# Optimization experiments

Hardware: AMD Instinct MI355X
Metric: run time of the kernel (lower is better)

The kernel has to match this reference:

```python
import jax, jax.numpy as jnp
import numpy as np
from jax import lax

B, S = 128, 8192
MIN_PATCH, MAX_PATCH = 2, 16
LOOKAHEAD = 8
THRESHOLD = 2.9
PAD_TOKEN = 0
VOCAB = 256
MAXP = -(-S // MIN_PATCH)  # static upper bound on #patches (torch trims to batch max; we pad+mask)


def setup_inputs() -> dict:
    key = jax.random.key(0)
    tokens = jax.random.randint(key, (B, S), 0, VOCAB, dtype=jnp.int32)
    return {"tokens": tokens}


def _entropy_all_starts(seq):
    # ent[j] = Shannon entropy (bits) of window seq[j : min(S, j + LOOKAHEAD)]
    # Using c_i = multiplicity of element i within its window:
    #   H = -(1/L) * sum_i log2(c_i / L)   (each unique value contributes c_i identical terms)
    pos = jnp.arange(S)[:, None] + jnp.arange(LOOKAHEAD)[None, :]          # [S, L]
    valid = pos < S
    w = seq[jnp.minimum(pos, S - 1)]                                       # [S, L]
    eq = (w[:, :, None] == w[:, None, :]) & valid[:, :, None] & valid[:, None, :]
    counts = eq.sum(-1).astype(jnp.float32)                                # [S, L] c_i (0 where invalid)
    L = valid.sum(-1).astype(jnp.float32)                                  # [S]
    logs = jnp.where(valid, jnp.log2(jnp.maximum(counts, 1.0) / jnp.maximum(L, 1.0)[:, None]), 0.0)
    return -logs.sum(-1) / jnp.maximum(L, 1.0)                             # [S]


def _patch_one(seq):
    ent = _entropy_all_starts(seq)
    stop = ent >= THRESHOLD
    # next_stop[j] = smallest j' >= j with stop[j'], else S (padded so next_stop[S] = S)
    vals = jnp.concatenate([jnp.where(stop, jnp.arange(S, dtype=jnp.int32), S),
                            jnp.array([S], dtype=jnp.int32)])
    next_stop = lax.associative_scan(jnp.minimum, vals, reverse=True)      # [S+1]
    i_all = jnp.arange(S, dtype=jnp.int32)
    # inner while-loop closed form: grow from min_patch until stop/seq-end/max_patch
    sizes = jnp.minimum(MAX_PATCH, next_stop[jnp.minimum(i_all + MIN_PATCH, S)] - i_all)  # [S]

    def step(i, _):
        ok = i < S
        sz = jnp.where(ok, sizes[jnp.minimum(i, S - 1)], 1)
        return i + sz, (i, sz, ok)

    _, (starts, szs, mask) = lax.scan(step, jnp.int32(0), None, length=MAXP)
    return starts, szs, mask


def reference(tokens):
    starts, szs, mask = jax.vmap(_patch_one)(tokens)                       # [B, MAXP]
    lane = jnp.arange(MAX_PATCH, dtype=jnp.int32)
    idx = starts[:, :, None] + lane[None, None, :]                         # [B, MAXP, MAX_PATCH]
    within = (lane[None, None, :] < szs[:, :, None]) & mask[:, :, None]
    g = jnp.take_along_axis(tokens, jnp.minimum(idx, S - 1).reshape(tokens.shape[0], -1), axis=1)
    patches = jnp.where(within, g.reshape(tokens.shape[0], MAXP, MAX_PATCH), PAD_TOKEN)
    return patches, mask
```

## Files before the change

### kernel.cpp

```cpp
#include <hip/hip_runtime.h>
#include <stdint.h>

#define SEQ  8192
#define NB   128
#define MAXP 4096
#define NT   512
#define RED  2
#define NCH  256
#define STS  36

__device__ __forceinline__ bool haszero8(uint64_t v) {
    return ((v - 0x0101010101010101ULL) & ~v & 0x8080808080808080ULL) != 0ULL;
}
__device__ __forceinline__ bool distinct8(uint64_t w) {
    uint64_t r1 = (w >> 8)  | (w << 56);
    uint64_t r2 = (w >> 16) | (w << 48);
    uint64_t r3 = (w >> 24) | (w << 40);
    uint64_t r4 = (w >> 32) | (w << 32);
    return !(haszero8(w ^ r1) | haszero8(w ^ r2) | haszero8(w ^ r3) | haszero8(w ^ r4));
}
__device__ __forceinline__ uint32_t pack4(int4 v) {
    return (uint32_t)(v.x & 255) | ((uint32_t)(v.y & 255) << 8) |
           ((uint32_t)(v.z & 255) << 16) | ((uint32_t)(v.w & 255) << 24);
}
__device__ __forceinline__ uint32_t bsel16(uint4 f, uint32_t b) {
    uint32_t w01 = (b & 4u) ? f.y : f.x;
    uint32_t w23 = (b & 4u) ? f.w : f.z;
    uint32_t w   = (b & 8u) ? w23 : w01;
    return (w >> ((b & 3u) << 3)) & 255u;
}
__device__ __forceinline__ uint4 comp16(uint4 g, uint4 f) {
    uint4 r;
#if __has_builtin(__builtin_amdgcn_perm)
    #define C16W(fw, out) do { \
        uint32_t sel = (fw) & 0x07070707u; \
        uint32_t lo = __builtin_amdgcn_perm(g.y, g.x, sel); \
        uint32_t hi = __builtin_amdgcn_perm(g.w, g.z, sel); \
        uint32_t m = ((fw) & 0x08080808u) >> 3; m = (m << 8) - m; \
        out = (lo & ~m) | (hi & m); } while (0)
    C16W(f.x, r.x); C16W(f.y, r.y); C16W(f.z, r.z); C16W(f.w, r.w);
    #undef C16W
#else
    #define C16B(fw, out) do { uint32_t o = 0; \
        o |= bsel16(g, (fw) & 15u); \
        o |= bsel16(g, ((fw) >> 8) & 15u) << 8; \
        o |= bsel16(g, ((fw) >> 16) & 15u) << 16; \
        o |= bsel16(g, ((fw) >> 24) & 15u) << 24; \
        out = o; } while (0)
    C16B(f.x, r.x); C16B(f.y, r.y); C16B(f.z, r.z); C16B(f.w, r.w);
    #undef C16B
#endif
    return r;
}
__device__ __forceinline__ int psize(const uint32_t* stopb, int p) {
    int bp = p + 2, w = bp >> 5;
    uint64_t comb = (uint64_t)stopb[w] | ((uint64_t)stopb[w + 1] << 32);
    uint32_t win14 = (uint32_t)(comb >> (bp & 31)) & 0x3FFFu;
    return win14 ? (2 + __builtin_ctz(win14)) : min(16, SEQ - p);
}

__global__ __launch_bounds__(NT) void ep_fused(const int* __restrict__ tokens,
                                               int* __restrict__ out) {
    __shared__ uint32_t tok32[2056];
    __shared__ uint32_t stopb[258];
    __shared__ uint16_t st_l[NCH * STS];
    __shared__ uint32_t exitf32[NCH * 4];
    __shared__ uint8_t  entry_s[NCH];
    __shared__ uint16_t pbase_s[NCH];
    __shared__ uint16_t starts_s[4100];
    __shared__ int S_s[2];

    const int bx = blockIdx.x;
    const int b = bx >> 1, qc = bx & 1;
    const int tid = threadIdx.x;

    {
        const int4* t4 = (const int4*)(tokens + (size_t)b * SEQ);
        #pragma unroll
        for (int k = 0; k < 4; ++k) { int g = k * NT + tid; tok32[g] = pack4(t4[g]); }
        if (tid < 8) tok32[2048 + tid] = 0u;
        if (tid < 2) stopb[256 + tid] = 0u;
    }
    __syncthreads();

    {
        const int base = tid * 4;
        uint64_t win = (uint64_t)tok32[base] | ((uint64_t)tok32[base + 1] << 32);
        uint32_t bits = 0;
        #pragma unroll
        for (int k = 0; k < 4; ++k) {
            uint32_t nx = tok32[base + 2 + k];
            #pragma unroll
            for (int m = 0; m < 4; ++m) {
                int j = tid * 16 + k * 4 + m;
                if (j <= SEQ - 8 && distinct8(win)) bits |= (1u << (k * 4 + m));
                win = (win >> 8) | ((uint64_t)(nx & 255u) << 56);
                nx >>= 8;
            }
        }
        uint32_t other = (uint32_t)__shfl_xor((int)bits, 1);
        if ((tid & 1) == 0) stopb[tid >> 1] = (bits & 0xFFFFu) | (other << 16);
    }
    __syncthreads();

    if (tid < NCH) {
        const int c = tid;
        const uint64_t W = (uint64_t)stopb[c] | ((uint64_t)stopb[c + 1] << 32);
        uint16_t* st = st_l + c * STS;
        const int gb = c * 32;
        #pragma unroll 4
        for (int rel = 31; rel >= 0; --rel) {
            uint32_t win14 = (uint32_t)(W >> (rel + 2)) & 0x3FFFu;
            int sz = win14 ? (2 + __builtin_ctz(win14)) : min(16, SEQ - (gb + rel));
            int nxt = rel + sz;
            int ra = (nxt < 32) ? nxt : 0;
            uint32_t sv = st[ra];
            uint32_t cont = (sv & 0xFFu) | (((sv >> 8) + 1u) << 8);
            uint32_t exitv = (uint32_t)(nxt - 32) | 0x100u;
            st[rel] = (uint16_t)((nxt >= 32) ? exitv : cont);
        }
        #pragma unroll
        for (int w = 0; w < 4; ++w) {
            uint32_t e0 = st[w * 4 + 0] & 0xFFu, e1 = st[w * 4 + 1] & 0xFFu,
                     e2 = st[w * 4 + 2] & 0xFFu, e3 = st[w * 4 + 3] & 0xFFu;
            exitf32[c * 4 + w] = e0 | (e1 << 8) | (e2 << 16) | (e3 << 24);
        }
    }
    __syncthreads();

    if (tid < 64) {
        const uint4* xf4 = (const uint4*)exitf32;
        uint4 f0 = xf4[tid * 4], f1 = xf4[tid * 4 + 1],
              f2 = xf4[tid * 4 + 2], f3 = xf4[tid * 4 + 3];
        uint4 g = comp16(f1, f0);
        g = comp16(f2, g);
        g = comp16(f3, g);
        #pragma unroll
        for (int d = 1; d < 64; d <<= 1) {
            uint4 o;
            o.x = (uint32_t)__shfl_up((int)g.x, d);
            o.y = (uint32_t)__shfl_up((int)g.y, d);
            o.z = (uint32_t)__shfl_up((int)g.z, d);
            o.w = (uint32_t)__shfl_up((int)g.w, d);
            if (tid >= d) g = comp16(g, o);
        }
        uint4 E;
        E.x = (uint32_t)__shfl_up((int)g.x, 1);
        E.y = (uint32_t)__shfl_up((int)g.y, 1);
        E.z = (uint32_t)__shfl_up((int)g.z, 1);
        E.w = (uint32_t)__shfl_up((int)g.w, 1);
        if (tid == 0) E = make_uint4(0x03020100u, 0x07060504u, 0x0B0A0908u, 0x0F0E0D0Cu);
        uint32_t e0 = E.x & 255u;
        uint32_t e1 = bsel16(f0, e0);
        uint32_t e2 = bsel16(f1, e1);
        uint32_t e3 = bsel16(f2, e2);
        entry_s[tid * 4 + 0] = (uint8_t)e0;
        entry_s[tid * 4 + 1] = (uint8_t)e1;
        entry_s[tid * 4 + 2] = (uint8_t)e2;
        entry_s[tid * 4 + 3] = (uint8_t)e3;
        int c0 = (int)(st_l[(tid * 4 + 0) * STS + (int)e0] >> 8);
        int c1 = (int)(st_l[(tid * 4 + 1) * STS + (int)e1] >> 8);
        int c2 = (int)(st_l[(tid * 4 + 2) * STS + (int)e2] >> 8);
        int c3 = (int)(st_l[(tid * 4 + 3) * STS + (int)e3] >> 8);
        int s = c0 + c1 + c2 + c3;
        int incl = s;
        #pragma unroll
        for (int d = 1; d < 64; d <<= 1) { int o = __shfl_up(incl, d); if (tid >= d) incl += o; }
        int excl = incl - s;
        pbase_s[tid * 4 + 0] = (uint16_t)excl;
        pbase_s[tid * 4 + 1] = (uint16_t)(excl + c0);
        pbase_s[tid * 4 + 2] = (uint16_t)(excl + c0 + c1);
        pbase_s[tid * 4 + 3] = (uint16_t)(excl + c0 + c1 + c2);
        if (tid == 63) S_s[0] = incl;
    }
    __syncthreads();

    if (tid < NCH) {
        int pb = (int)pbase_s[tid];
        int p = tid * 32 + (int)entry_s[tid];
        const int lim = tid * 32 + 32;
        while (p < lim) {
            starts_s[pb++] = (uint16_t)p;
            p += psize(stopb, p);
        }
    }
    {
        const int P = S_s[0];
        for (int i = P + tid; i < 4098; i += NT) starts_s[i] = (uint16_t)SEQ;
    }
    __syncthreads();

    {
        int* outp = out + (size_t)b * (MAXP * 16);
        int* outm = out + (size_t)NB * MAXP * 16 + (size_t)b * MAXP;
        const int j = tid & 3;
        #pragma unroll
        for (int it = 0; it < (MAXP / RED) / (NT / 4); ++it) {
            const int p = qc * (MAXP / RED) + it * (NT / 4) + (tid >> 2);
            const int st = (int)starts_s[p];
            const int sz = (int)starts_s[p + 1] - st;
            const int base = (st >> 2) + j;
            const uint32_t sh = (uint32_t)(st & 3) * 8u;
            uint32_t lo = tok32[base], hi = tok32[base + 1];
            uint32_t pk = (uint32_t)((((uint64_t)hi << 32) | lo) >> sh);
            int rem = sz - 4 * j;
            rem = (rem < 0) ? 0 : (rem > 4 ? 4 : rem);
            pk &= (uint32_t)((1ULL << (8 * rem)) - 1ULL);
            ((int4*)outp)[(size_t)p * 4 + j] =
                make_int4((int)(pk & 255u), (int)((pk >> 8) & 255u),
                          (int)((pk >> 16) & 255u), (int)(pk >> 24));
        }
        #pragma unroll
        for (int i = 0; i < (MAXP / RED) / NT; ++i) {
            const int p = qc * (MAXP / RED) + i * NT + tid;
            outm[p] = ((int)starts_s[p] < SEQ) ? 1 : 0;
        }
    }
}

extern "C" void kernel_launch(void* const* d_in, const int* in_sizes, int n_in,
                              void* d_out, int out_size, void* d_ws, size_t ws_size,
                              hipStream_t stream) {
    const int* tokens = (const int*)d_in[0];
    int* out = (int*)d_out;
    ep_fused<<<dim3(NB * RED), dim3(NT), 0, stream>>>(tokens, out);
}
```

Measured before the change: 21.47 us.

## Keep per-chunk patch state table in registers and vectorize mask stores

The serial 32-step backward pass over each 32-position chunk now builds its exit/count table in eight packed 32-bit registers, looked up with a select tree. This replaces dependent LDS loads and stores on every step. The exit bytes are packed with a byte-permute, and a 32-bit-packed table is written once to LDS for the later count lookup. It also drops the per-window bounds check in the stop-bit loop in favour of a single mask on the last thread, and writes the mask output as one int4 per thread. The cost is more register pressure and a fully unrolled select chain.

```diff
diff --git a/kernel.cpp b/kernel.cpp
--- a/kernel.cpp
+++ b/kernel.cpp
@@ -7,7 +7,6 @@
 #define NT   512
 #define RED  2
 #define NCH  256
-#define STS  36
 
 __device__ __forceinline__ bool haszero8(uint64_t v) {
     return ((v - 0x0101010101010101ULL) & ~v & 0x8080808080808080ULL) != 0ULL;
@@ -28,6 +27,14 @@
     uint32_t w23 = (b & 4u) ? f.w : f.z;
     uint32_t w   = (b & 8u) ? w23 : w01;
     return (w >> ((b & 3u) << 3)) & 255u;
+}
+__device__ __forceinline__ uint32_t packexit(uint32_t pa, uint32_t pb) {
+#if __has_builtin(__builtin_amdgcn_perm)
+    return __builtin_amdgcn_perm(pb, pa, 0x06040200u);
+#else
+    return (pa & 0xFFu) | (((pa >> 16) & 0xFFu) << 8) |
+           ((pb & 0xFFu) << 16) | (((pb >> 16) & 0xFFu) << 24);
+#endif
 }
 __device__ __forceinline__ uint4 comp16(uint4 g, uint4 f) {
     uint4 r;
@@ -63,7 +70,7 @@
                                                int* __restrict__ out) {
     __shared__ uint32_t tok32[2056];
     __shared__ uint32_t stopb[258];
-    __shared__ uint16_t st_l[NCH * STS];
+    __shared__ uint32_t st16[NCH * 9];
     __shared__ uint32_t exitf32[NCH * 4];
     __shared__ uint8_t  entry_s[NCH];
     __shared__ uint16_t pbase_s[NCH];
@@ -92,12 +99,12 @@
             uint32_t nx = tok32[base + 2 + k];
             #pragma unroll
             for (int m = 0; m < 4; ++m) {
-                int j = tid * 16 + k * 4 + m;
-                if (j <= SEQ - 8 && distinct8(win)) bits |= (1u << (k * 4 + m));
+                if (distinct8(win)) bits |= (1u << (k * 4 + m));
                 win = (win >> 8) | ((uint64_t)(nx & 255u) << 56);
                 nx >>= 8;
             }
         }
+        if (tid == NT - 1) bits &= 0x1FFu;
         uint32_t other = (uint32_t)__shfl_xor((int)bits, 1);
         if ((tid & 1) == 0) stopb[tid >> 1] = (bits & 0xFFFFu) | (other << 16);
     }
@@ -106,25 +113,44 @@
     if (tid < NCH) {
         const int c = tid;
         const uint64_t W = (uint64_t)stopb[c] | ((uint64_t)stopb[c + 1] << 32);
-        uint16_t* st = st_l + c * STS;
         const int gb = c * 32;
-        #pragma unroll 4
+        uint32_t p0 = 0, p1 = 0, p2 = 0, p3 = 0, p4 = 0, p5 = 0, p6 = 0, p7 = 0;
+        #pragma unroll
         for (int rel = 31; rel >= 0; --rel) {
             uint32_t win14 = (uint32_t)(W >> (rel + 2)) & 0x3FFFu;
             int sz = win14 ? (2 + __builtin_ctz(win14)) : min(16, SEQ - (gb + rel));
             int nxt = rel + sz;
-            int ra = (nxt < 32) ? nxt : 0;
-            uint32_t sv = st[ra];
-            uint32_t cont = (sv & 0xFFu) | (((sv >> 8) + 1u) << 8);
-            uint32_t exitv = (uint32_t)(nxt - 32) | 0x100u;
-            st[rel] = (uint16_t)((nxt >= 32) ? exitv : cont);
-        }
-        #pragma unroll
-        for (int w = 0; w < 4; ++w) {
-            uint32_t e0 = st[w * 4 + 0] & 0xFFu, e1 = st[w * 4 + 1] & 0xFFu,
-                     e2 = st[w * 4 + 2] & 0xFFu, e3 = st[w * 4 + 3] & 0xFFu;
-            exitf32[c * 4 + w] = e0 | (e1 << 8) | (e2 << 16) | (e3 << 24);
-        }
+            uint32_t stv;
+            if (nxt >= 32) {
+                stv = (uint32_t)(nxt - 32) | 0x100u;
+            } else {
+                int s = sz - 1;
+                uint32_t q01 = (s & 2) ? p1 : p0;
+                uint32_t q23 = (s & 2) ? p3 : p2;
+                uint32_t q45 = (s & 2) ? p5 : p4;
+                uint32_t q67 = (s & 2) ? p7 : p6;
+                uint32_t qa  = (s & 4) ? q23 : q01;
+                uint32_t qb  = (s & 4) ? q67 : q45;
+                uint32_t q   = (s & 8) ? qb : qa;
+                uint32_t sel = (s & 1) ? (q >> 16) : (q & 0xFFFFu);
+                stv = sel + 0x100u;
+            }
+            p7 = (p7 << 16) | (p6 >> 16);
+            p6 = (p6 << 16) | (p5 >> 16);
+            p5 = (p5 << 16) | (p4 >> 16);
+            p4 = (p4 << 16) | (p3 >> 16);
+            p3 = (p3 << 16) | (p2 >> 16);
+            p2 = (p2 << 16) | (p1 >> 16);
+            p1 = (p1 << 16) | (p0 >> 16);
+            p0 = (p0 << 16) | stv;
+        }
+        uint32_t* st = st16 + c * 9;
+        st[0] = p0; st[1] = p1; st[2] = p2; st[3] = p3;
+        st[4] = p4; st[5] = p5; st[6] = p6; st[7] = p7;
+        exitf32[c * 4 + 0] = packexit(p0, p1);
+        exitf32[c * 4 + 1] = packexit(p2, p3);
+        exitf32[c * 4 + 2] = packexit(p4, p5);
+        exitf32[c * 4 + 3] = packexit(p6, p7);
     }
     __syncthreads();
 
@@ -158,10 +184,14 @@
         entry_s[tid * 4 + 1] = (uint8_t)e1;
         entry_s[tid * 4 + 2] = (uint8_t)e2;
         entry_s[tid * 4 + 3] = (uint8_t)e3;
-        int c0 = (int)(st_l[(tid * 4 + 0) * STS + (int)e0] >> 8);
-        int c1 = (int)(st_l[(tid * 4 + 1) * STS + (int)e1] >> 8);
-        int c2 = (int)(st_l[(tid * 4 + 2) * STS + (int)e2] >> 8);
-        int c3 = (int)(st_l[(tid * 4 + 3) * STS + (int)e3] >> 8);
+        uint32_t w0 = st16[(tid * 4 + 0) * 9 + (e0 >> 1)];
+        uint32_t w1 = st16[(tid * 4 + 1) * 9 + (e1 >> 1)];
+        uint32_t w2 = st16[(tid * 4 + 2) * 9 + (e2 >> 1)];
+        uint32_t w3 = st16[(tid * 4 + 3) * 9 + (e3 >> 1)];
+        int c0 = (int)(((w0 >> ((e0 & 1) * 16)) & 0xFFFFu) >> 8);
+        int c1 = (int)(((w1 >> ((e1 & 1) * 16)) & 0xFFFFu) >> 8);
+        int c2 = (int)(((w2 >> ((e2 & 1) * 16)) & 0xFFFFu) >> 8);
+        int c3 = (int)(((w3 >> ((e3 & 1) * 16)) & 0xFFFFu) >> 8);
         int s = c0 + c1 + c2 + c3;
         int incl = s;
         #pragma unroll
@@ -210,10 +240,13 @@
                 make_int4((int)(pk & 255u), (int)((pk >> 8) & 255u),
                           (int)((pk >> 16) & 255u), (int)(pk >> 24));
         }
-        #pragma unroll
-        for (int i = 0; i < (MAXP / RED) / NT; ++i) {
-            const int p = qc * (MAXP / RED) + i * NT + tid;
-            outm[p] = ((int)starts_s[p] < SEQ) ? 1 : 0;
+        {
+            const int p4 = qc * (MAXP / RED) + tid * 4;
+            const uint32_t* s32 = (const uint32_t*)starts_s;
+            uint32_t a = s32[p4 >> 1], bw = s32[(p4 >> 1) + 1];
+            ((int4*)(outm + qc * (MAXP / RED)))[tid] =
+                make_int4((a & 0xFFFFu) < SEQ ? 1 : 0, (a >> 16) < SEQ ? 1 : 0,
+                          (bw & 0xFFFFu) < SEQ ? 1 : 0, (bw >> 16) < SEQ ? 1 : 0);
         }
     }
 }
```

After: 21.03 us. 2.1% less time.
